# Kernel tuning notes

Hardware: AMD Instinct MI355X
Metric: run time of the kernel (lower is better)

Reference implementation:

```python
import jax, jax.numpy as jnp
import numpy as np

B, O, L, N, V, H = 4, 4, 128, 8, 256, 256  # batch, options, max_len, topN, vec_size, hidden


def _gru(x, wih, whh, bih, bhh):
    """PyTorch-style GRU (gate order r,z,n), zero init hidden. x: [b,t,d] -> [b,t,H]."""
    xg = jnp.einsum('btd,gd->btg', x, wih) + bih  # input projections for all steps
    h0 = jnp.zeros((x.shape[0], whh.shape[1]), x.dtype)

    def step(h, xt):
        hg = h @ whh.T + bhh
        xr, xz, xn = jnp.split(xt, 3, axis=-1)
        hr, hz, hn = jnp.split(hg, 3, axis=-1)
        r = jax.nn.sigmoid(xr + hr)
        z = jax.nn.sigmoid(xz + hz)
        n = jnp.tanh(xn + r * hn)
        h = (1.0 - z) * n + z * h
        return h, h

    _, ys = jax.lax.scan(step, h0, jnp.swapaxes(xg, 0, 1))
    return jnp.swapaxes(ys, 0, 1)


def setup_inputs() -> dict:
    key = jax.random.key(0)
    ks = jax.random.split(key, 19)
    r = lambda k, s, sc=1.0: jax.random.normal(k, s, jnp.float32) * sc
    w = 0.05  # weight scale
    return {
        'statement': r(ks[0], (B, L, V)),
        'answer': r(ks[1], (B, O, L, V)),
        'refs': r(ks[2], (B, O, N, L, V)),
        'ctx_wih': r(ks[3], (3 * H, V), w), 'ctx_whh': r(ks[4], (3 * H, H), w),
        'ctx_bih': r(ks[5], (3 * H,), w), 'ctx_bhh': r(ks[6], (3 * H,), w),
        'sr_wih': r(ks[7], (3 * H, H), w), 'sr_whh': r(ks[8], (3 * H, H), w),
        'sr_bih': r(ks[9], (3 * H,), w), 'sr_bhh': r(ks[10], (3 * H,), w),
        'dr_wih': r(ks[11], (3 * H, 2 * H), w), 'dr_whh': r(ks[12], (3 * H, H), w),
        'dr_bih': r(ks[13], (3 * H,), w), 'dr_bhh': r(ks[14], (3 * H,), w),
        'gate_w': r(ks[15], (1, 2 * H), w), 'gate_b': r(ks[16], (1,), w),
        'out_w': r(ks[17], (1, 4 * H), w), 'out_b': r(ks[18], (1,), w),
    }


def reference(statement, answer, refs,
              ctx_wih, ctx_whh, ctx_bih, ctx_bhh,
              sr_wih, sr_whh, sr_bih, sr_bhh,
              dr_wih, dr_whh, dr_bih, dr_bhh,
              gate_w, gate_b, out_w, out_b):
    Ls = 2 * L
    # statement = cat(question, option) per option, context-encoded (option loop vectorized)
    q = jnp.broadcast_to(statement[:, None], (B, O, L, V))
    stmt = jnp.concatenate([q, answer], axis=2)  # [B,O,Ls,V]
    stmt = _gru(stmt.reshape(B * O, Ls, V), ctx_wih, ctx_whh, ctx_bih, ctx_bhh).reshape(B, O, Ls, H)
    docs = _gru(refs.reshape(B * O * N, L, V), ctx_wih, ctx_whh, ctx_bih, ctx_bhh).reshape(B, O, N, L, H)
    # statement-doc co-attention (doc loop vectorized)
    match = jnp.einsum('bosh,bonlh->bonsl', stmt, docs)  # [B,O,N,Ls,L]
    read_sum = jnp.einsum('bonsl,bonlh->bonsh', jax.nn.softmax(match, axis=-1), docs)  # [B,O,N,Ls,H]
    doc_read = jnp.einsum('bonsl,bosh->bonlh', jax.nn.softmax(match, axis=3), stmt)    # [B,O,N,L,H]
    dri = jnp.concatenate([docs, doc_read], axis=-1)  # [B,O,N,L,2H]
    # doc-doc cross attention against all topN*L positions
    flat = dri.reshape(B, O, N * L, 2 * H)
    mm = jnp.einsum('bonld,bomd->bonlm', dri, flat)  # [B,O,N,L,N*L]
    att = jnp.einsum('bonlm,bomd->bonld', jax.nn.softmax(mm, axis=-1), flat)  # [B,O,N,L,2H]
    # reasoning GRUs + max-pool over time
    s_r = _gru(read_sum.reshape(B * O * N, Ls, H), sr_wih, sr_whh, sr_bih, sr_bhh).max(axis=1).reshape(B, O, N, H)
    d_r = _gru(att.reshape(B * O * N, L, 2 * H), dr_wih, dr_whh, dr_bih, dr_bhh).max(axis=1).reshape(B, O, N, H)
    res = jnp.concatenate([s_r, d_r], axis=-1)  # [B,O,N,2H]
    coef = jnp.einsum('bond,ed->bone', res, gate_w) + gate_b  # [B,O,N,1] (no sigmoid, as in source)
    res = coef * res
    feat = jnp.concatenate([res.max(axis=2), res.mean(axis=2)], axis=-1)  # [B,O,4H]
    out = jnp.einsum('bod,ed->boe', feat, out_w)[..., 0] + out_b  # [B,O]
    return jax.nn.softmax(out, axis=1)
```

## Files before the change

### kernel.cpp

```cpp
#include <hip/hip_runtime.h>
#include <hip/hip_bf16.h>
#include <hip/hip_fp16.h>


typedef unsigned short u16;
typedef unsigned int u32;
typedef __attribute__((ext_vector_type(8))) short short8;
typedef __attribute__((ext_vector_type(4))) float floatx4;

__device__ __forceinline__ float bf2f(u16 v) { return __uint_as_float(((u32)v) << 16); }
__device__ __forceinline__ u16 f2b(float f) {
  u32 u = __float_as_uint(f);
  return (u16)((u + 0x7fffu + ((u >> 16) & 1u)) >> 16);
}
__device__ __forceinline__ float ldf(u16 v) { return bf2f(v); }
__device__ __forceinline__ float ldf(float v) { return v; }
__device__ __forceinline__ void stf(u16* p, float v) { *p = f2b(v); }
__device__ __forceinline__ void stf(float* p, float v) { *p = v; }
__device__ __forceinline__ float ldraw(const void* p, size_t i, int isf) {
  return isf ? ((const float*)p)[i] : bf2f(((const u16*)p)[i]);
}
__device__ __forceinline__ __half2 u2h(u32 v) {
  union { u32 u; __half2 h; } c; c.u = v; return c.h;
}

__global__ void k_detect(const void* __restrict__ stmt, int* __restrict__ flag) {
  if (threadIdx.x == 0 && blockIdx.x == 0) {
    const float* f = (const float*)stmt;
    int sane = 0;
    for (int i = 0; i < 64; ++i) {
      const float a = fabsf(f[i]);
      if (a > 1e-20f && a < 1e6f) sane++;
    }
    *flag = (sane >= 48) ? 1 : 0;
  }
}

__global__ __launch_bounds__(256) void k_cvt(const void* __restrict__ in, u16* __restrict__ out,
                                             int n, const int* __restrict__ flag) {
  const int isf = *flag;
  const int i = blockIdx.x * 256 + threadIdx.x;
  if (i < n) out[i] = f2b(ldraw(in, i, isf));
}

__global__ __launch_bounds__(256) void k_gather_stmt(const void* __restrict__ statement,
                                                     const void* __restrict__ answer,
                                                     u16* __restrict__ out,
                                                     const int* __restrict__ flag) {
  const int isf = *flag;
  const int idx = blockIdx.x * 256 + threadIdx.x;
  const int v = idx & 255;
  const int s = (idx >> 8) & 255;
  const int bo = idx >> 16;
  float val;
  if (s < 128) val = ldraw(statement, (size_t)(((bo >> 2) * 128) + s) * 256 + v, isf);
  else         val = ldraw(answer, (size_t)((bo * 128) + (s - 128)) * 256 + v, isf);
  out[idx] = f2b(val);
}

__global__ __launch_bounds__(256) void k_packh(const void* __restrict__ in, u32* __restrict__ out,
                                               int total, const int* __restrict__ flag) {
  const int isf = *flag;
  const int idx = blockIdx.x * 256 + threadIdx.x;
  if (idx >= total) return;
  const int r = idx % 768;
  const int k2 = idx / 768;
  const float a = ldraw(in, (size_t)r * 256 + 2 * k2, isf);
  const float b = ldraw(in, (size_t)r * 256 + 2 * k2 + 1, isf);
  const __half2 h2 = __floats2half2_rn(a, b);
  out[(((size_t)(k2 >> 2) * 768) + r) * 4 + (k2 & 3)] = *reinterpret_cast<const u32*>(&h2);
}

#define LOADW(i) uint4 w##i = wp[(i) * 768];
#define PINW(i) asm volatile("" : "+v"(w##i.x), "+v"(w##i.y), "+v"(w##i.z), "+v"(w##i.w));
#define STEPW(i)                                                             \
  {                                                                          \
    const uint4 hv = *reinterpret_cast<const uint4*>(&hs_h[(i) * 8]);        \
    a0 = __hfma2(u2h(w##i.x), u2h(hv.x), a0);                                \
    a1 = __hfma2(u2h(w##i.y), u2h(hv.y), a1);                                \
    a2 = __hfma2(u2h(w##i.z), u2h(hv.z), a2);                                \
    a3 = __hfma2(u2h(w##i.w), u2h(hv.w), a3);                                \
  }

__global__ __attribute__((amdgpu_flat_work_group_size(768, 768), amdgpu_waves_per_eu(3, 3)))
void k_rec(
    const u16* __restrict__ xg0, const u32* __restrict__ whh0,
    const u16* __restrict__ bih0, const u16* __restrict__ bhh0,
    u16* __restrict__ oseq0, float* __restrict__ omax0, int nseq0, int T0,
    const u16* __restrict__ xg1, const u32* __restrict__ whh1,
    const u16* __restrict__ bih1, const u16* __restrict__ bhh1,
    u16* __restrict__ oseq1, float* __restrict__ omax1, int T1) {
  __shared__ __align__(16) char smem[82176];
  float* hs_f = reinterpret_cast<float*>(smem);
  __half* hs_h = reinterpret_cast<__half*>(smem + 1024);
  float* sh = reinterpret_cast<float*>(smem + 2048);
  const u16 *xg, *bih, *bhh; const u32* whh; u16* oseq; float* omax; int T, seq;
  if ((int)blockIdx.x < nseq0) {
    seq = blockIdx.x; xg = xg0; whh = whh0; bih = bih0; bhh = bhh0;
    oseq = oseq0; omax = omax0; T = T0;
  } else {
    seq = blockIdx.x - nseq0; xg = xg1; whh = whh1; bih = bih1; bhh = bhh1;
    oseq = oseq1; omax = omax1; T = T1;
  }
  const int t = threadIdx.x;
  const uint4* wp = reinterpret_cast<const uint4*>(whh) + t;
  LOADW(0)  LOADW(1)  LOADW(2)  LOADW(3)  LOADW(4)  LOADW(5)  LOADW(6)  LOADW(7)
  LOADW(8)  LOADW(9)  LOADW(10) LOADW(11) LOADW(12) LOADW(13) LOADW(14) LOADW(15)
  LOADW(16) LOADW(17) LOADW(18) LOADW(19) LOADW(20) LOADW(21) LOADW(22) LOADW(23)
  LOADW(24) LOADW(25) LOADW(26) LOADW(27) LOADW(28) LOADW(29) LOADW(30) LOADW(31)
  PINW(0)  PINW(1)  PINW(2)  PINW(3)  PINW(4)  PINW(5)  PINW(6)  PINW(7)
  PINW(8)  PINW(9)  PINW(10) PINW(11) PINW(12) PINW(13) PINW(14) PINW(15)
  PINW(16) PINW(17) PINW(18) PINW(19) PINW(20) PINW(21) PINW(22) PINW(23)
  PINW(24) PINW(25) PINW(26) PINW(27) PINW(28) PINW(29) PINW(30) PINW(31)
  const float bh = bf2f(bhh[t]);
  float bir = 0.f, biz = 0.f, bin = 0.f;
  if (t < 256) {
    bir = bf2f(bih[t]); biz = bf2f(bih[t + 256]); bin = bf2f(bih[t + 512]);
    hs_f[t] = 0.f;
    hs_h[t] = __float2half(0.f);
  }
  float vmax = -3.4e38f;
  const u16* xrow = xg + (size_t)seq * T * 768;
  for (int st = 0; st < T; ++st, xrow += 768) {
    float xr = 0.f, xz = 0.f, xn = 0.f;
    if (t < 256) {
      xr = bf2f(xrow[t]); xz = bf2f(xrow[t + 256]); xn = bf2f(xrow[t + 512]);
    }
    __syncthreads();
    __half2 a0 = __floats2half2_rn(0.f, 0.f), a1 = a0, a2 = a0, a3 = a0;
    STEPW(0)  STEPW(1)  STEPW(2)  STEPW(3)  STEPW(4)  STEPW(5)  STEPW(6)  STEPW(7)
    STEPW(8)  STEPW(9)  STEPW(10) STEPW(11) STEPW(12) STEPW(13) STEPW(14) STEPW(15)
    STEPW(16) STEPW(17) STEPW(18) STEPW(19) STEPW(20) STEPW(21) STEPW(22) STEPW(23)
    STEPW(24) STEPW(25) STEPW(26) STEPW(27) STEPW(28) STEPW(29) STEPW(30) STEPW(31)
    const float ah = (__low2float(a0) + __high2float(a0)) + (__low2float(a1) + __high2float(a1))
                   + (__low2float(a2) + __high2float(a2)) + (__low2float(a3) + __high2float(a3));
    sh[t] = ah + bh;
    __syncthreads();
    if (t < 256) {
      const float r = 1.f / (1.f + __expf(-(xr + bir + sh[t])));
      const float z = 1.f / (1.f + __expf(-(xz + biz + sh[t + 256])));
      const float n = tanhf(xn + bin + r * sh[t + 512]);
      const float hnew = (1.f - z) * n + z * hs_f[t];
      hs_f[t] = hnew;
      hs_h[t] = __float2half(hnew);
      if (oseq) oseq[(size_t)(seq * T + st) * 256 + t] = f2b(hnew);
      vmax = fmaxf(vmax, hnew);
    }
  }
  if (omax && t < 256) omax[(size_t)seq * 256 + t] = vmax;
}

template <bool BT, bool CADD, typename TA, typename TB, typename TC>
__global__ __launch_bounds__(256) void k_mgemm(
    const TA* __restrict__ Abase, int lda, long strideA, int divA,
    const TB* __restrict__ Bbase, int ldb, long strideB, int divB,
    TC* __restrict__ Cbase, int ldc, long strideC, int K) {
  const int z = blockIdx.z;
  const TA* A = Abase + (size_t)(z / divA) * strideA;
  const TB* Bp = Bbase + (size_t)(z / divB) * strideB;
  TC* C = Cbase + (size_t)z * strideC;
  const int m0 = blockIdx.y << 6, n0 = blockIdx.x << 6;
  __shared__ __align__(16) u16 As[2048];
  __shared__ __align__(16) u16 Bs[2048];
  const int t = threadIdx.x;
  const int lane = t & 63, w = t >> 6;
  floatx4 acc0 = {0.f, 0.f, 0.f, 0.f};
  floatx4 acc1 = {0.f, 0.f, 0.f, 0.f};
  floatx4 acc2 = {0.f, 0.f, 0.f, 0.f};
  floatx4 acc3 = {0.f, 0.f, 0.f, 0.f};
  const int ar = t >> 2;
  const int ac = (t & 3) << 3;
  const int adst = (((ar >> 4) << 6) | (ar & 15) | ((t & 3) << 4)) << 3;
  const int bk = t >> 3;
  const int bn = (t & 7) << 3;
  for (int k0 = 0; k0 < K; k0 += 32) {
    {
      const TA* ap = A + (size_t)(m0 + ar) * lda + (k0 + ac);
      if constexpr (sizeof(TA) == 2) {
        *reinterpret_cast<uint4*>(&As[adst]) = *reinterpret_cast<const uint4*>(ap);
      } else {
        const float4 f0 = reinterpret_cast<const float4*>(ap)[0];
        const float4 f1 = reinterpret_cast<const float4*>(ap)[1];
        u16* d = &As[adst];
        d[0] = f2b(f0.x); d[1] = f2b(f0.y); d[2] = f2b(f0.z); d[3] = f2b(f0.w);
        d[4] = f2b(f1.x); d[5] = f2b(f1.y); d[6] = f2b(f1.z); d[7] = f2b(f1.w);
      }
    }
    if constexpr (BT) {
      const TB* bp = Bp + (size_t)(n0 + ar) * ldb + (k0 + ac);
      *reinterpret_cast<uint4*>(&Bs[adst]) = *reinterpret_cast<const uint4*>(bp);
    } else {
      const TB* bp = Bp + (size_t)(k0 + bk) * ldb + (n0 + bn);
      const uint4 v = *reinterpret_cast<const uint4*>(bp);
      const u16* pv = reinterpret_cast<const u16*>(&v);
#pragma unroll
      for (int j = 0; j < 8; ++j) {
        const int n = bn + j;
        Bs[(((((n >> 4) << 6) | (n & 15) | ((bk >> 3) << 4)) << 3) | (bk & 7))] = pv[j];
      }
    }
    __syncthreads();
    const short8 af = *reinterpret_cast<const short8*>(&As[(w * 64 + lane) << 3]);
    const short8 b0 = *reinterpret_cast<const short8*>(&Bs[(lane) << 3]);
    const short8 b1 = *reinterpret_cast<const short8*>(&Bs[(64 + lane) << 3]);
    const short8 b2 = *reinterpret_cast<const short8*>(&Bs[(128 + lane) << 3]);
    const short8 b3 = *reinterpret_cast<const short8*>(&Bs[(192 + lane) << 3]);
    acc0 = __builtin_amdgcn_mfma_f32_16x16x32_bf16(af, b0, acc0, 0, 0, 0);
    acc1 = __builtin_amdgcn_mfma_f32_16x16x32_bf16(af, b1, acc1, 0, 0, 0);
    acc2 = __builtin_amdgcn_mfma_f32_16x16x32_bf16(af, b2, acc2, 0, 0, 0);
    acc3 = __builtin_amdgcn_mfma_f32_16x16x32_bf16(af, b3, acc3, 0, 0, 0);
    __syncthreads();
  }
  const int q = lane >> 4, cn = lane & 15;
  TC* crow = C + (size_t)(m0 + (w << 4) + (q << 2)) * ldc + n0 + cn;
#pragma unroll
  for (int i = 0; i < 4; ++i) {
    TC* cp = crow + (size_t)i * ldc;
    float v0 = acc0[i], v1 = acc1[i], v2 = acc2[i], v3 = acc3[i];
    if (CADD) { v0 += ldf(cp[0]); v1 += ldf(cp[16]); v2 += ldf(cp[32]); v3 += ldf(cp[48]); }
    stf(cp + 0, v0); stf(cp + 16, v1); stf(cp + 32, v2); stf(cp + 48, v3);
  }
}

template <typename TI, typename TO>
__global__ __launch_bounds__(256) void k_softmax_row(const TI* __restrict__ in,
                                                     TO* __restrict__ out, int Lrow) {
  const TI* p = in + (size_t)blockIdx.x * Lrow;
  TO* q = out + (size_t)blockIdx.x * Lrow;
  const int t = threadIdx.x;
  __shared__ float redA[4];
  __shared__ float redB[4];
  float m = -3.4e38f;
  for (int i = t; i < Lrow; i += 256) m = fmaxf(m, ldf(p[i]));
  for (int o = 32; o; o >>= 1) m = fmaxf(m, __shfl_xor(m, o, 64));
  if ((t & 63) == 0) redA[t >> 6] = m;
  __syncthreads();
  m = fmaxf(fmaxf(redA[0], redA[1]), fmaxf(redA[2], redA[3]));
  float s = 0.f;
  for (int i = t; i < Lrow; i += 256) {
    const float e = __expf(ldf(p[i]) - m);
    stf(q + i, e);
    s += e;
  }
  for (int o = 32; o; o >>= 1) s += __shfl_xor(s, o, 64);
  if ((t & 63) == 0) redB[t >> 6] = s;
  __syncthreads();
  s = redB[0] + redB[1] + redB[2] + redB[3];
  const float inv = 1.f / s;
  for (int i = t; i < Lrow; i += 256) stf(q + i, ldf(q[i]) * inv);
}

__global__ __launch_bounds__(256) void k_softmax_colT(const float* __restrict__ match,
                                                      u16* __restrict__ qT) {
  const int bon = blockIdx.x, l = blockIdx.y;
  const int t = threadIdx.x;
  __shared__ float redA[4];
  __shared__ float redB[4];
  const float x = match[((size_t)bon * 256 + t) * 128 + l];
  float m = x;
  for (int o = 32; o; o >>= 1) m = fmaxf(m, __shfl_xor(m, o, 64));
  if ((t & 63) == 0) redA[t >> 6] = m;
  __syncthreads();
  m = fmaxf(fmaxf(redA[0], redA[1]), fmaxf(redA[2], redA[3]));
  const float e = __expf(x - m);
  float s = e;
  for (int o = 32; o; o >>= 1) s += __shfl_xor(s, o, 64);
  if ((t & 63) == 0) redB[t >> 6] = s;
  __syncthreads();
  s = redB[0] + redB[1] + redB[2] + redB[3];
  qT[((size_t)bon * 128 + l) * 256 + t] = f2b(e / s);
}

__global__ __launch_bounds__(256) void k_final(
    const float* __restrict__ s_r, const float* __restrict__ d_r,
    const u16* __restrict__ gw, const u16* __restrict__ gb,
    const u16* __restrict__ ow, const u16* __restrict__ ob,
    void* __restrict__ out, const int* __restrict__ flag) {
  __shared__ float coef[128];
  __shared__ float logits[16];
  const int t = threadIdx.x;
  if (t < 128) {
    float acc = bf2f(gb[0]);
    const float* sp = s_r + (size_t)t * 256;
    const float* dp = d_r + (size_t)t * 256;
    for (int d = 0; d < 256; ++d) acc += bf2f(gw[d]) * sp[d];
    for (int d = 0; d < 256; ++d) acc += bf2f(gw[256 + d]) * dp[d];
    coef[t] = acc;
  }
  __syncthreads();
  if (t < 16) {
    float acc = bf2f(ob[0]);
    for (int d = 0; d < 512; ++d) {
      float mx = -3.4e38f, sm = 0.f;
      for (int n = 0; n < 8; ++n) {
        const int bon = t * 8 + n;
        const float base = (d < 256) ? s_r[(size_t)bon * 256 + d] : d_r[(size_t)bon * 256 + (d - 256)];
        const float v = coef[bon] * base;
        mx = fmaxf(mx, v);
        sm += v;
      }
      acc += bf2f(ow[d]) * mx + bf2f(ow[512 + d]) * (sm * 0.125f);
    }
    logits[t] = acc;
  }
  __syncthreads();
  if (t < 4) {
    const int isf = *flag;
    float m = -3.4e38f;
    for (int o = 0; o < 4; ++o) m = fmaxf(m, logits[t * 4 + o]);
    float e[4], s = 0.f;
    for (int o = 0; o < 4; ++o) { e[o] = __expf(logits[t * 4 + o] - m); s += e[o]; }
    for (int o = 0; o < 4; ++o) {
      const float v = e[o] / s;
      if (isf) ((float*)out)[t * 4 + o] = v;
      else     ((u16*)out)[t * 4 + o] = f2b(v);
    }
  }
}

extern "C" void kernel_launch(void* const* d_in, const int* in_sizes, int n_in,
                              void* d_out, int out_size, void* d_ws, size_t ws_size,
                              hipStream_t stream) {
  (void)in_sizes; (void)n_in; (void)out_size; (void)ws_size;
  const void* statement = d_in[0];
  const void* answer    = d_in[1];
  const void* refs      = d_in[2];
  const void* ctx_wih = d_in[3];
  const void* ctx_whh = d_in[4];
  const void* ctx_bih = d_in[5];
  const void* ctx_bhh = d_in[6];
  const void* sr_wih = d_in[7];
  const void* sr_whh = d_in[8];
  const void* sr_bih = d_in[9];
  const void* sr_bhh = d_in[10];
  const void* dr_wih = d_in[11];
  const void* dr_whh = d_in[12];
  const void* dr_bih = d_in[13];
  const void* dr_bhh = d_in[14];
  const void* gate_w = d_in[15];
  const void* gate_b = d_in[16];
  const void* out_w  = d_in[17];
  const void* out_b  = d_in[18];

  char* ws = (char*)d_ws;
  size_t off = 0;
  auto alloc = [&](size_t bytes) -> void* {
    void* p = ws + off;
    off += (bytes + 255) & ~(size_t)255;
    return p;
  };
  int* FLAG    = (int*)alloc(256);
  u16* CTXWIH  = (u16*)alloc((size_t)768 * 256 * 2);
  u16* SRWIH   = (u16*)alloc((size_t)768 * 256 * 2);
  u16* DRWIH   = (u16*)alloc((size_t)768 * 512 * 2);
  u32* CTXWHH2 = (u32*)alloc((size_t)128 * 768 * 4);
  u32* SRWHH2  = (u32*)alloc((size_t)128 * 768 * 4);
  u32* DRWHH2  = (u32*)alloc((size_t)128 * 768 * 4);
  u16* B_CTX_I = (u16*)alloc(768 * 2);
  u16* B_CTX_H = (u16*)alloc(768 * 2);
  u16* B_SR_I  = (u16*)alloc(768 * 2);
  u16* B_SR_H  = (u16*)alloc(768 * 2);
  u16* B_DR_I  = (u16*)alloc(768 * 2);
  u16* B_DR_H  = (u16*)alloc(768 * 2);
  u16* GW = (u16*)alloc(512 * 2);
  u16* GB = (u16*)alloc(2);
  u16* OW = (u16*)alloc(1024 * 2);
  u16* OB = (u16*)alloc(2);
  u16* STMT_H   = (u16*)alloc((size_t)16 * 256 * 256 * 2);
  u16* DOCS_H   = (u16*)alloc((size_t)128 * 128 * 256 * 2);
  u16* DOC_READ = (u16*)alloc((size_t)128 * 128 * 256 * 2);
  u16* ATT      = (u16*)alloc((size_t)128 * 128 * 512 * 2);
  float* SR_R = (float*)alloc((size_t)128 * 256 * 4);
  float* DR_R = (float*)alloc((size_t)128 * 256 * 4);
  const size_t ovl = off;
  u16* REFS_B   = (u16*)(ws + ovl);
  u16* STMT_IN  = (u16*)(ws + ovl + ((size_t)8 << 20));
  u16* XG_DOCS  = (u16*)(ws + ovl + ((size_t)16 << 20));
  u16* XG_STMT  = (u16*)(ws + ovl + ((size_t)41 << 20));
  float* MATCH  = (float*)(ws + ovl);
  u16* P_ROW    = (u16*)(ws + ovl + ((size_t)16 << 20));
  u16* MATCH_Q  = (u16*)(ws + ovl + ((size_t)24 << 20));
  u16* READ_SUM = (u16*)(ws + ovl + ((size_t)50 << 20));
  u16* XG_SR    = (u16*)(ws + ovl);
  float* MM     = (float*)(ws + ovl);
  u16* XG_DR    = (u16*)(ws + ovl);

  k_detect<<<1, 64, 0, stream>>>(statement, FLAG);

  k_gather_stmt<<<4096, 256, 0, stream>>>(statement, answer, STMT_IN, FLAG);
  k_cvt<<<16384, 256, 0, stream>>>(refs, REFS_B, 4194304, FLAG);
  k_cvt<<<768, 256, 0, stream>>>(ctx_wih, CTXWIH, 196608, FLAG);
  k_cvt<<<768, 256, 0, stream>>>(sr_wih, SRWIH, 196608, FLAG);
  k_cvt<<<1536, 256, 0, stream>>>(dr_wih, DRWIH, 393216, FLAG);
  k_packh<<<384, 256, 0, stream>>>(ctx_whh, CTXWHH2, 98304, FLAG);
  k_packh<<<384, 256, 0, stream>>>(sr_whh, SRWHH2, 98304, FLAG);
  k_packh<<<384, 256, 0, stream>>>(dr_whh, DRWHH2, 98304, FLAG);
  k_cvt<<<3, 256, 0, stream>>>(ctx_bih, B_CTX_I, 768, FLAG);
  k_cvt<<<3, 256, 0, stream>>>(ctx_bhh, B_CTX_H, 768, FLAG);
  k_cvt<<<3, 256, 0, stream>>>(sr_bih, B_SR_I, 768, FLAG);
  k_cvt<<<3, 256, 0, stream>>>(sr_bhh, B_SR_H, 768, FLAG);
  k_cvt<<<3, 256, 0, stream>>>(dr_bih, B_DR_I, 768, FLAG);
  k_cvt<<<3, 256, 0, stream>>>(dr_bhh, B_DR_H, 768, FLAG);
  k_cvt<<<2, 256, 0, stream>>>(gate_w, GW, 512, FLAG);
  k_cvt<<<1, 256, 0, stream>>>(gate_b, GB, 1, FLAG);
  k_cvt<<<4, 256, 0, stream>>>(out_w, OW, 1024, FLAG);
  k_cvt<<<1, 256, 0, stream>>>(out_b, OB, 1, FLAG);

  k_mgemm<true, false, u16, u16, u16><<<dim3(12, 64, 1), 256, 0, stream>>>(
      STMT_IN, 256, 0L, 1, CTXWIH, 256, 0L, 1, XG_STMT, 768, 0L, 256);
  k_mgemm<true, false, u16, u16, u16><<<dim3(12, 256, 1), 256, 0, stream>>>(
      REFS_B, 256, 0L, 1, CTXWIH, 256, 0L, 1, XG_DOCS, 768, 0L, 256);

  k_rec<<<144, 768, 0, stream>>>(
      XG_STMT, CTXWHH2, B_CTX_I, B_CTX_H, STMT_H, nullptr, 16, 256,
      XG_DOCS, CTXWHH2, B_CTX_I, B_CTX_H, DOCS_H, nullptr, 128);

  k_mgemm<true, false, u16, u16, float><<<dim3(2, 4, 128), 256, 0, stream>>>(
      STMT_H, 256, 65536L, 8, DOCS_H, 256, 32768L, 1, MATCH, 128, 32768L, 256);

  k_softmax_colT<<<dim3(128, 128), 256, 0, stream>>>(MATCH, MATCH_Q);
  k_softmax_row<float, u16><<<32768, 256, 0, stream>>>(MATCH, P_ROW, 128);

  k_mgemm<false, false, u16, u16, u16><<<dim3(4, 4, 128), 256, 0, stream>>>(
      P_ROW, 128, 32768L, 1, DOCS_H, 256, 32768L, 1, READ_SUM, 256, 65536L, 128);

  k_mgemm<false, false, u16, u16, u16><<<dim3(4, 2, 128), 256, 0, stream>>>(
      MATCH_Q, 256, 32768L, 1, STMT_H, 256, 65536L, 8, DOC_READ, 256, 32768L, 256);

  k_mgemm<true, false, u16, u16, u16><<<dim3(12, 512, 1), 256, 0, stream>>>(
      READ_SUM, 256, 0L, 1, SRWIH, 256, 0L, 1, XG_SR, 768, 0L, 256);

  k_rec<<<128, 768, 0, stream>>>(
      XG_SR, SRWHH2, B_SR_I, B_SR_H, nullptr, SR_R, 128, 256,
      nullptr, nullptr, nullptr, nullptr, nullptr, nullptr, 0);

  k_mgemm<true, false, u16, u16, float><<<dim3(16, 16, 16), 256, 0, stream>>>(
      DOCS_H, 256, 262144L, 1, DOCS_H, 256, 262144L, 1, MM, 1024, 1048576L, 256);
  k_mgemm<true, true, u16, u16, float><<<dim3(16, 16, 16), 256, 0, stream>>>(
      DOC_READ, 256, 262144L, 1, DOC_READ, 256, 262144L, 1, MM, 1024, 1048576L, 256);

  k_softmax_row<float, float><<<16384, 256, 0, stream>>>(MM, MM, 1024);

  k_mgemm<false, false, float, u16, u16><<<dim3(4, 16, 16), 256, 0, stream>>>(
      MM, 1024, 1048576L, 1, DOCS_H, 256, 262144L, 1, ATT, 512, 524288L, 1024);
  k_mgemm<false, false, float, u16, u16><<<dim3(4, 16, 16), 256, 0, stream>>>(
      MM, 1024, 1048576L, 1, DOC_READ, 256, 262144L, 1, ATT + 256, 512, 524288L, 1024);

  k_mgemm<true, false, u16, u16, u16><<<dim3(12, 256, 1), 256, 0, stream>>>(
      ATT, 512, 0L, 1, DRWIH, 512, 0L, 1, XG_DR, 768, 0L, 512);

  k_rec<<<128, 768, 0, stream>>>(
      XG_DR, DRWHH2, B_DR_I, B_DR_H, nullptr, DR_R, 128, 128,
      nullptr, nullptr, nullptr, nullptr, nullptr, nullptr, 0);

  k_final<<<1, 256, 0, stream>>>(SR_R, DR_R, GW, GB, OW, OB, d_out, FLAG);
}
```

Measured before the change: 1.714 ms.

## Remap GRU recurrence to 512 threads, each owning three gate rows over half the hidden dimension

The recurrent kernel now runs 512 threads instead of 768. Each thread keeps 48 packed fp16 weight vectors in registers, covering three consecutive W_hh rows over half of K. Thread pairs combine their partial sums with a lane shuffle, and the weight packing kernel is rewritten to match the new register layout. Each hidden-state vector read from LDS is now reused across three rows, which cuts LDS traffic and wave count per step. The cost is higher register pressure (192 VGPRs just for weights) and an extra shuffle and reduction on the serial per-step critical path.

```diff
diff --git a/kernel.cpp b/kernel.cpp
--- a/kernel.cpp
+++ b/kernel.cpp
@@ -61,28 +61,20 @@
 __global__ __launch_bounds__(256) void k_packh(const void* __restrict__ in, u32* __restrict__ out,
                                                int total, const int* __restrict__ flag) {
   const int isf = *flag;
-  const int idx = blockIdx.x * 256 + threadIdx.x;
-  if (idx >= total) return;
-  const int r = idx % 768;
-  const int k2 = idx / 768;
-  const float a = ldraw(in, (size_t)r * 256 + 2 * k2, isf);
-  const float b = ldraw(in, (size_t)r * 256 + 2 * k2 + 1, isf);
+  const int g = blockIdx.x * 256 + threadIdx.x;
+  if (g >= total) return;
+  const int i = g >> 11;
+  const int t = (g >> 2) & 511;
+  const int m = g & 3;
+  const int row = 3 * (t >> 1) + (i >> 4);
+  const int k = (t & 1) * 128 + (i & 15) * 8 + 2 * m;
+  const float a = ldraw(in, (size_t)row * 256 + k, isf);
+  const float b = ldraw(in, (size_t)row * 256 + k + 1, isf);
   const __half2 h2 = __floats2half2_rn(a, b);
-  out[(((size_t)(k2 >> 2) * 768) + r) * 4 + (k2 & 3)] = *reinterpret_cast<const u32*>(&h2);
-}
-
-#define LOADW(i) uint4 w##i = wp[(i) * 768];
-#define PINW(i) asm volatile("" : "+v"(w##i.x), "+v"(w##i.y), "+v"(w##i.z), "+v"(w##i.w));
-#define STEPW(i)                                                             \
-  {                                                                          \
-    const uint4 hv = *reinterpret_cast<const uint4*>(&hs_h[(i) * 8]);        \
-    a0 = __hfma2(u2h(w##i.x), u2h(hv.x), a0);                                \
-    a1 = __hfma2(u2h(w##i.y), u2h(hv.y), a1);                                \
-    a2 = __hfma2(u2h(w##i.z), u2h(hv.z), a2);                                \
-    a3 = __hfma2(u2h(w##i.w), u2h(hv.w), a3);                                \
-  }
-
-__global__ __attribute__((amdgpu_flat_work_group_size(768, 768), amdgpu_waves_per_eu(3, 3)))
+  out[g] = *reinterpret_cast<const u32*>(&h2);
+}
+
+__global__ __attribute__((amdgpu_flat_work_group_size(512, 512), amdgpu_waves_per_eu(2, 2)))
 void k_rec(
     const u16* __restrict__ xg0, const u32* __restrict__ whh0,
     const u16* __restrict__ bih0, const u16* __restrict__ bhh0,
@@ -90,10 +82,9 @@
     const u16* __restrict__ xg1, const u32* __restrict__ whh1,
     const u16* __restrict__ bih1, const u16* __restrict__ bhh1,
     u16* __restrict__ oseq1, float* __restrict__ omax1, int T1) {
-  __shared__ __align__(16) char smem[82176];
-  float* hs_f = reinterpret_cast<float*>(smem);
-  __half* hs_h = reinterpret_cast<__half*>(smem + 1024);
-  float* sh = reinterpret_cast<float*>(smem + 2048);
+  __shared__ __align__(16) float hs_f[256];
+  __shared__ __align__(16) __half hs_h[256];
+  __shared__ __align__(16) float sh[768];
   const u16 *xg, *bih, *bhh; const u32* whh; u16* oseq; float* omax; int T, seq;
   if ((int)blockIdx.x < nseq0) {
     seq = blockIdx.x; xg = xg0; whh = whh0; bih = bih0; bhh = bhh0;
@@ -103,22 +94,22 @@
     oseq = oseq1; omax = omax1; T = T1;
   }
   const int t = threadIdx.x;
+  const int p = t >> 1, kh = t & 1;
   const uint4* wp = reinterpret_cast<const uint4*>(whh) + t;
-  LOADW(0)  LOADW(1)  LOADW(2)  LOADW(3)  LOADW(4)  LOADW(5)  LOADW(6)  LOADW(7)
-  LOADW(8)  LOADW(9)  LOADW(10) LOADW(11) LOADW(12) LOADW(13) LOADW(14) LOADW(15)
-  LOADW(16) LOADW(17) LOADW(18) LOADW(19) LOADW(20) LOADW(21) LOADW(22) LOADW(23)
-  LOADW(24) LOADW(25) LOADW(26) LOADW(27) LOADW(28) LOADW(29) LOADW(30) LOADW(31)
-  PINW(0)  PINW(1)  PINW(2)  PINW(3)  PINW(4)  PINW(5)  PINW(6)  PINW(7)
-  PINW(8)  PINW(9)  PINW(10) PINW(11) PINW(12) PINW(13) PINW(14) PINW(15)
-  PINW(16) PINW(17) PINW(18) PINW(19) PINW(20) PINW(21) PINW(22) PINW(23)
-  PINW(24) PINW(25) PINW(26) PINW(27) PINW(28) PINW(29) PINW(30) PINW(31)
-  const float bh = bf2f(bhh[t]);
+  uint4 w[48];
+#pragma unroll
+  for (int i = 0; i < 48; ++i) w[i] = wp[i * 512];
+  float bh0 = 0.f, bh1 = 0.f, bh2 = 0.f;
+  if (!kh) {
+    bh0 = bf2f(bhh[3 * p]); bh1 = bf2f(bhh[3 * p + 1]); bh2 = bf2f(bhh[3 * p + 2]);
+  }
   float bir = 0.f, biz = 0.f, bin = 0.f;
   if (t < 256) {
     bir = bf2f(bih[t]); biz = bf2f(bih[t + 256]); bin = bf2f(bih[t + 512]);
     hs_f[t] = 0.f;
     hs_h[t] = __float2half(0.f);
   }
+  const uint4* hs4 = reinterpret_cast<const uint4*>(hs_h) + (kh << 4);
   float vmax = -3.4e38f;
   const u16* xrow = xg + (size_t)seq * T * 768;
   for (int st = 0; st < T; ++st, xrow += 768) {
@@ -127,14 +118,38 @@
       xr = bf2f(xrow[t]); xz = bf2f(xrow[t + 256]); xn = bf2f(xrow[t + 512]);
     }
     __syncthreads();
-    __half2 a0 = __floats2half2_rn(0.f, 0.f), a1 = a0, a2 = a0, a3 = a0;
-    STEPW(0)  STEPW(1)  STEPW(2)  STEPW(3)  STEPW(4)  STEPW(5)  STEPW(6)  STEPW(7)
-    STEPW(8)  STEPW(9)  STEPW(10) STEPW(11) STEPW(12) STEPW(13) STEPW(14) STEPW(15)
-    STEPW(16) STEPW(17) STEPW(18) STEPW(19) STEPW(20) STEPW(21) STEPW(22) STEPW(23)
-    STEPW(24) STEPW(25) STEPW(26) STEPW(27) STEPW(28) STEPW(29) STEPW(30) STEPW(31)
-    const float ah = (__low2float(a0) + __high2float(a0)) + (__low2float(a1) + __high2float(a1))
-                   + (__low2float(a2) + __high2float(a2)) + (__low2float(a3) + __high2float(a3));
-    sh[t] = ah + bh;
+#pragma unroll
+    for (int i = 0; i < 48; ++i)
+      asm volatile("" : "+v"(w[i].x), "+v"(w[i].y), "+v"(w[i].z), "+v"(w[i].w));
+    const __half2 z2 = __floats2half2_rn(0.f, 0.f);
+    __half2 a00 = z2, a01 = z2, a10 = z2, a11 = z2, a20 = z2, a21 = z2;
+#pragma unroll
+    for (int c = 0; c < 16; ++c) {
+      const uint4 hv = hs4[c];
+      a00 = __hfma2(u2h(w[c].x),      u2h(hv.x), a00);
+      a01 = __hfma2(u2h(w[c].y),      u2h(hv.y), a01);
+      a00 = __hfma2(u2h(w[c].z),      u2h(hv.z), a00);
+      a01 = __hfma2(u2h(w[c].w),      u2h(hv.w), a01);
+      a10 = __hfma2(u2h(w[16 + c].x), u2h(hv.x), a10);
+      a11 = __hfma2(u2h(w[16 + c].y), u2h(hv.y), a11);
+      a10 = __hfma2(u2h(w[16 + c].z), u2h(hv.z), a10);
+      a11 = __hfma2(u2h(w[16 + c].w), u2h(hv.w), a11);
+      a20 = __hfma2(u2h(w[32 + c].x), u2h(hv.x), a20);
+      a21 = __hfma2(u2h(w[32 + c].y), u2h(hv.y), a21);
+      a20 = __hfma2(u2h(w[32 + c].z), u2h(hv.z), a20);
+      a21 = __hfma2(u2h(w[32 + c].w), u2h(hv.w), a21);
+    }
+    float s0 = (__low2float(a00) + __high2float(a00)) + (__low2float(a01) + __high2float(a01));
+    float s1 = (__low2float(a10) + __high2float(a10)) + (__low2float(a11) + __high2float(a11));
+    float s2 = (__low2float(a20) + __high2float(a20)) + (__low2float(a21) + __high2float(a21));
+    s0 += __shfl_xor(s0, 1, 64);
+    s1 += __shfl_xor(s1, 1, 64);
+    s2 += __shfl_xor(s2, 1, 64);
+    if (!kh) {
+      sh[3 * p]     = s0 + bh0;
+      sh[3 * p + 1] = s1 + bh1;
+      sh[3 * p + 2] = s2 + bh2;
+    }
     __syncthreads();
     if (t < 256) {
       const float r = 1.f / (1.f + __expf(-(xr + bir + sh[t])));
@@ -411,7 +426,7 @@
   k_mgemm<true, false, u16, u16, u16><<<dim3(12, 256, 1), 256, 0, stream>>>(
       REFS_B, 256, 0L, 1, CTXWIH, 256, 0L, 1, XG_DOCS, 768, 0L, 256);
 
-  k_rec<<<144, 768, 0, stream>>>(
+  k_rec<<<144, 512, 0, stream>>>(
       XG_STMT, CTXWHH2, B_CTX_I, B_CTX_H, STMT_H, nullptr, 16, 256,
       XG_DOCS, CTXWHH2, B_CTX_I, B_CTX_H, DOCS_H, nullptr, 128);
 
@@ -430,7 +445,7 @@
   k_mgemm<true, false, u16, u16, u16><<<dim3(12, 512, 1), 256, 0, stream>>>(
       READ_SUM, 256, 0L, 1, SRWIH, 256, 0L, 1, XG_SR, 768, 0L, 256);
 
-  k_rec<<<128, 768, 0, stream>>>(
+  k_rec<<<128, 512, 0, stream>>>(
       XG_SR, SRWHH2, B_SR_I, B_SR_H, nullptr, SR_R, 128, 256,
       nullptr, nullptr, nullptr, nullptr, nullptr, nullptr, 0);
 
@@ -449,7 +464,7 @@
   k_mgemm<true, false, u16, u16, u16><<<dim3(12, 256, 1), 256, 0, stream>>>(
       ATT, 512, 0L, 1, DRWIH, 512, 0L, 1, XG_DR, 768, 0L, 512);
 
-  k_rec<<<128, 768, 0, stream>>>(
+  k_rec<<<128, 512, 0, stream>>>(
       XG_DR, DRWHH2, B_DR_I, B_DR_H, nullptr, DR_R, 128, 128,
       nullptr, nullptr, nullptr, nullptr, nullptr, nullptr, 0);
 
```

Measured after the change: 1.737 ms. Within noise of the previous version (+1.4%).

## Process two GRU sequences per block, streaming recurrent weights from cache

Applied to the files above, without the earlier changes.

The recurrent GRU kernel now lets each 768-thread block advance two independent sequences at once. Each weight vector is loaded once per step and applied to both hidden states, and the gate math is split across thread ranges. The old scheme pinned all recurrent weights in registers with a waves-per-EU hint. That is dropped, so weights are re-read from L1/L2 on every step, and launches shrink to roughly half as many blocks. This trades register-resident weights for fewer, busier blocks, with added per-step load latency and less parallelism across CUs.

```diff
diff --git a/kernel.cpp b/kernel.cpp
--- a/kernel.cpp
+++ b/kernel.cpp
@@ -71,83 +71,126 @@
   out[(((size_t)(k2 >> 2) * 768) + r) * 4 + (k2 & 3)] = *reinterpret_cast<const u32*>(&h2);
 }
 
-#define LOADW(i) uint4 w##i = wp[(i) * 768];
-#define PINW(i) asm volatile("" : "+v"(w##i.x), "+v"(w##i.y), "+v"(w##i.z), "+v"(w##i.w));
-#define STEPW(i)                                                             \
-  {                                                                          \
-    const uint4 hv = *reinterpret_cast<const uint4*>(&hs_h[(i) * 8]);        \
-    a0 = __hfma2(u2h(w##i.x), u2h(hv.x), a0);                                \
-    a1 = __hfma2(u2h(w##i.y), u2h(hv.y), a1);                                \
-    a2 = __hfma2(u2h(w##i.z), u2h(hv.z), a2);                                \
-    a3 = __hfma2(u2h(w##i.w), u2h(hv.w), a3);                                \
-  }
-
-__global__ __attribute__((amdgpu_flat_work_group_size(768, 768), amdgpu_waves_per_eu(3, 3)))
+#define HH1(i)                                                              \
+  {                                                                         \
+    const uint4 wv = wp[(i) * 768];                                         \
+    const uint4 hA = *reinterpret_cast<const uint4*>(&hsA_h[(i) * 8]);      \
+    a0 = __hfma2(u2h(wv.x), u2h(hA.x), a0);                                 \
+    a1 = __hfma2(u2h(wv.y), u2h(hA.y), a1);                                 \
+    a2 = __hfma2(u2h(wv.z), u2h(hA.z), a2);                                 \
+    a3 = __hfma2(u2h(wv.w), u2h(hA.w), a3);                                 \
+  }
+#define HH2(i)                                                              \
+  {                                                                         \
+    const uint4 wv = wp[(i) * 768];                                         \
+    const uint4 hA = *reinterpret_cast<const uint4*>(&hsA_h[(i) * 8]);      \
+    const uint4 hB = *reinterpret_cast<const uint4*>(&hsB_h[(i) * 8]);      \
+    a0 = __hfma2(u2h(wv.x), u2h(hA.x), a0);                                 \
+    a1 = __hfma2(u2h(wv.y), u2h(hA.y), a1);                                 \
+    a2 = __hfma2(u2h(wv.z), u2h(hA.z), a2);                                 \
+    a3 = __hfma2(u2h(wv.w), u2h(hA.w), a3);                                 \
+    b0 = __hfma2(u2h(wv.x), u2h(hB.x), b0);                                 \
+    b1 = __hfma2(u2h(wv.y), u2h(hB.y), b1);                                 \
+    b2 = __hfma2(u2h(wv.z), u2h(hB.z), b2);                                 \
+    b3 = __hfma2(u2h(wv.w), u2h(hB.w), b3);                                 \
+  }
+
+__global__ __attribute__((amdgpu_flat_work_group_size(768, 768)))
 void k_rec(
     const u16* __restrict__ xg0, const u32* __restrict__ whh0,
     const u16* __restrict__ bih0, const u16* __restrict__ bhh0,
-    u16* __restrict__ oseq0, float* __restrict__ omax0, int nseq0, int T0,
+    u16* __restrict__ oseq0, float* __restrict__ omax0, int nblk0, int S0, int T0,
     const u16* __restrict__ xg1, const u32* __restrict__ whh1,
     const u16* __restrict__ bih1, const u16* __restrict__ bhh1,
-    u16* __restrict__ oseq1, float* __restrict__ omax1, int T1) {
-  __shared__ __align__(16) char smem[82176];
-  float* hs_f = reinterpret_cast<float*>(smem);
-  __half* hs_h = reinterpret_cast<__half*>(smem + 1024);
-  float* sh = reinterpret_cast<float*>(smem + 2048);
-  const u16 *xg, *bih, *bhh; const u32* whh; u16* oseq; float* omax; int T, seq;
-  if ((int)blockIdx.x < nseq0) {
-    seq = blockIdx.x; xg = xg0; whh = whh0; bih = bih0; bhh = bhh0;
-    oseq = oseq0; omax = omax0; T = T0;
+    u16* __restrict__ oseq1, float* __restrict__ omax1, int S1, int T1) {
+  __shared__ __align__(16) float hsA_f[256];
+  __shared__ __align__(16) float hsB_f[256];
+  __shared__ __align__(16) __half hsA_h[256];
+  __shared__ __align__(16) __half hsB_h[256];
+  __shared__ __align__(16) float shA[768];
+  __shared__ __align__(16) float shB[768];
+  const u16 *xg, *bih, *bhh; const u32* whh; u16* oseq; float* omax; int T, S, blk;
+  if ((int)blockIdx.x < nblk0) {
+    blk = blockIdx.x; xg = xg0; whh = whh0; bih = bih0; bhh = bhh0;
+    oseq = oseq0; omax = omax0; T = T0; S = S0;
   } else {
-    seq = blockIdx.x - nseq0; xg = xg1; whh = whh1; bih = bih1; bhh = bhh1;
-    oseq = oseq1; omax = omax1; T = T1;
+    blk = blockIdx.x - nblk0; xg = xg1; whh = whh1; bih = bih1; bhh = bhh1;
+    oseq = oseq1; omax = omax1; T = T1; S = S1;
   }
   const int t = threadIdx.x;
+  const bool dual = (S == 2);
+  const int seqA = blk * S;
   const uint4* wp = reinterpret_cast<const uint4*>(whh) + t;
-  LOADW(0)  LOADW(1)  LOADW(2)  LOADW(3)  LOADW(4)  LOADW(5)  LOADW(6)  LOADW(7)
-  LOADW(8)  LOADW(9)  LOADW(10) LOADW(11) LOADW(12) LOADW(13) LOADW(14) LOADW(15)
-  LOADW(16) LOADW(17) LOADW(18) LOADW(19) LOADW(20) LOADW(21) LOADW(22) LOADW(23)
-  LOADW(24) LOADW(25) LOADW(26) LOADW(27) LOADW(28) LOADW(29) LOADW(30) LOADW(31)
-  PINW(0)  PINW(1)  PINW(2)  PINW(3)  PINW(4)  PINW(5)  PINW(6)  PINW(7)
-  PINW(8)  PINW(9)  PINW(10) PINW(11) PINW(12) PINW(13) PINW(14) PINW(15)
-  PINW(16) PINW(17) PINW(18) PINW(19) PINW(20) PINW(21) PINW(22) PINW(23)
-  PINW(24) PINW(25) PINW(26) PINW(27) PINW(28) PINW(29) PINW(30) PINW(31)
   const float bh = bf2f(bhh[t]);
   float bir = 0.f, biz = 0.f, bin = 0.f;
   if (t < 256) {
     bir = bf2f(bih[t]); biz = bf2f(bih[t + 256]); bin = bf2f(bih[t + 512]);
-    hs_f[t] = 0.f;
-    hs_h[t] = __float2half(0.f);
+    hsA_f[t] = 0.f; hsA_h[t] = __float2half(0.f);
+  } else if (dual && t < 512) {
+    const int e = t - 256;
+    bir = bf2f(bih[e]); biz = bf2f(bih[e + 256]); bin = bf2f(bih[e + 512]);
+    hsB_f[e] = 0.f; hsB_h[e] = __float2half(0.f);
   }
   float vmax = -3.4e38f;
-  const u16* xrow = xg + (size_t)seq * T * 768;
-  for (int st = 0; st < T; ++st, xrow += 768) {
+  const u16* xrowA = xg + (size_t)seqA * T * 768;
+  const u16* xrowB = xg + (size_t)(seqA + 1) * T * 768;
+  for (int st = 0; st < T; ++st, xrowA += 768, xrowB += 768) {
     float xr = 0.f, xz = 0.f, xn = 0.f;
     if (t < 256) {
-      xr = bf2f(xrow[t]); xz = bf2f(xrow[t + 256]); xn = bf2f(xrow[t + 512]);
+      xr = bf2f(xrowA[t]); xz = bf2f(xrowA[t + 256]); xn = bf2f(xrowA[t + 512]);
+    } else if (dual && t < 512) {
+      const int e = t - 256;
+      xr = bf2f(xrowB[e]); xz = bf2f(xrowB[e + 256]); xn = bf2f(xrowB[e + 512]);
     }
     __syncthreads();
-    __half2 a0 = __floats2half2_rn(0.f, 0.f), a1 = a0, a2 = a0, a3 = a0;
-    STEPW(0)  STEPW(1)  STEPW(2)  STEPW(3)  STEPW(4)  STEPW(5)  STEPW(6)  STEPW(7)
-    STEPW(8)  STEPW(9)  STEPW(10) STEPW(11) STEPW(12) STEPW(13) STEPW(14) STEPW(15)
-    STEPW(16) STEPW(17) STEPW(18) STEPW(19) STEPW(20) STEPW(21) STEPW(22) STEPW(23)
-    STEPW(24) STEPW(25) STEPW(26) STEPW(27) STEPW(28) STEPW(29) STEPW(30) STEPW(31)
-    const float ah = (__low2float(a0) + __high2float(a0)) + (__low2float(a1) + __high2float(a1))
+    const __half2 z2 = __floats2half2_rn(0.f, 0.f);
+    __half2 a0 = z2, a1 = z2, a2 = z2, a3 = z2;
+    __half2 b0 = z2, b1 = z2, b2 = z2, b3 = z2;
+    if (dual) {
+      HH2(0)  HH2(1)  HH2(2)  HH2(3)  HH2(4)  HH2(5)  HH2(6)  HH2(7)
+      HH2(8)  HH2(9)  HH2(10) HH2(11) HH2(12) HH2(13) HH2(14) HH2(15)
+      HH2(16) HH2(17) HH2(18) HH2(19) HH2(20) HH2(21) HH2(22) HH2(23)
+      HH2(24) HH2(25) HH2(26) HH2(27) HH2(28) HH2(29) HH2(30) HH2(31)
+    } else {
+      HH1(0)  HH1(1)  HH1(2)  HH1(3)  HH1(4)  HH1(5)  HH1(6)  HH1(7)
+      HH1(8)  HH1(9)  HH1(10) HH1(11) HH1(12) HH1(13) HH1(14) HH1(15)
+      HH1(16) HH1(17) HH1(18) HH1(19) HH1(20) HH1(21) HH1(22) HH1(23)
+      HH1(24) HH1(25) HH1(26) HH1(27) HH1(28) HH1(29) HH1(30) HH1(31)
+    }
+    const float sA = (__low2float(a0) + __high2float(a0)) + (__low2float(a1) + __high2float(a1))
                    + (__low2float(a2) + __high2float(a2)) + (__low2float(a3) + __high2float(a3));
-    sh[t] = ah + bh;
+    shA[t] = sA + bh;
+    if (dual) {
+      const float sB = (__low2float(b0) + __high2float(b0)) + (__low2float(b1) + __high2float(b1))
+                     + (__low2float(b2) + __high2float(b2)) + (__low2float(b3) + __high2float(b3));
+      shB[t] = sB + bh;
+    }
     __syncthreads();
     if (t < 256) {
-      const float r = 1.f / (1.f + __expf(-(xr + bir + sh[t])));
-      const float z = 1.f / (1.f + __expf(-(xz + biz + sh[t + 256])));
-      const float n = tanhf(xn + bin + r * sh[t + 512]);
-      const float hnew = (1.f - z) * n + z * hs_f[t];
-      hs_f[t] = hnew;
-      hs_h[t] = __float2half(hnew);
-      if (oseq) oseq[(size_t)(seq * T + st) * 256 + t] = f2b(hnew);
+      const float r = 1.f / (1.f + __expf(-(xr + bir + shA[t])));
+      const float z = 1.f / (1.f + __expf(-(xz + biz + shA[t + 256])));
+      const float n = tanhf(xn + bin + r * shA[t + 512]);
+      const float hnew = (1.f - z) * n + z * hsA_f[t];
+      hsA_f[t] = hnew;
+      hsA_h[t] = __float2half(hnew);
+      if (oseq) oseq[(size_t)(seqA * T + st) * 256 + t] = f2b(hnew);
       vmax = fmaxf(vmax, hnew);
-    }
-  }
-  if (omax && t < 256) omax[(size_t)seq * 256 + t] = vmax;
+    } else if (dual && t < 512) {
+      const int e = t - 256;
+      const float r = 1.f / (1.f + __expf(-(xr + bir + shB[e])));
+      const float z = 1.f / (1.f + __expf(-(xz + biz + shB[e + 256])));
+      const float n = tanhf(xn + bin + r * shB[e + 512]);
+      const float hnew = (1.f - z) * n + z * hsB_f[e];
+      hsB_f[e] = hnew;
+      hsB_h[e] = __float2half(hnew);
+      if (oseq) oseq[(size_t)((seqA + 1) * T + st) * 256 + e] = f2b(hnew);
+      vmax = fmaxf(vmax, hnew);
+    }
+  }
+  if (omax) {
+    if (t < 256) omax[(size_t)seqA * 256 + t] = vmax;
+    else if (dual && t < 512) omax[(size_t)(seqA + 1) * 256 + (t - 256)] = vmax;
+  }
 }
 
 template <bool BT, bool CADD, typename TA, typename TB, typename TC>
@@ -411,9 +454,9 @@
   k_mgemm<true, false, u16, u16, u16><<<dim3(12, 256, 1), 256, 0, stream>>>(
       REFS_B, 256, 0L, 1, CTXWIH, 256, 0L, 1, XG_DOCS, 768, 0L, 256);
 
-  k_rec<<<144, 768, 0, stream>>>(
-      XG_STMT, CTXWHH2, B_CTX_I, B_CTX_H, STMT_H, nullptr, 16, 256,
-      XG_DOCS, CTXWHH2, B_CTX_I, B_CTX_H, DOCS_H, nullptr, 128);
+  k_rec<<<80, 768, 0, stream>>>(
+      XG_STMT, CTXWHH2, B_CTX_I, B_CTX_H, STMT_H, nullptr, 16, 1, 256,
+      XG_DOCS, CTXWHH2, B_CTX_I, B_CTX_H, DOCS_H, nullptr, 2, 128);
 
   k_mgemm<true, false, u16, u16, float><<<dim3(2, 4, 128), 256, 0, stream>>>(
       STMT_H, 256, 65536L, 8, DOCS_H, 256, 32768L, 1, MATCH, 128, 32768L, 256);
@@ -430,9 +473,9 @@
   k_mgemm<true, false, u16, u16, u16><<<dim3(12, 512, 1), 256, 0, stream>>>(
       READ_SUM, 256, 0L, 1, SRWIH, 256, 0L, 1, XG_SR, 768, 0L, 256);
 
-  k_rec<<<128, 768, 0, stream>>>(
-      XG_SR, SRWHH2, B_SR_I, B_SR_H, nullptr, SR_R, 128, 256,
-      nullptr, nullptr, nullptr, nullptr, nullptr, nullptr, 0);
+  k_rec<<<64, 768, 0, stream>>>(
+      XG_SR, SRWHH2, B_SR_I, B_SR_H, nullptr, SR_R, 64, 2, 256,
+      nullptr, nullptr, nullptr, nullptr, nullptr, nullptr, 0, 0);
 
   k_mgemm<true, false, u16, u16, float><<<dim3(16, 16, 16), 256, 0, stream>>>(
       DOCS_H, 256, 262144L, 1, DOCS_H, 256, 262144L, 1, MM, 1024, 1048576L, 256);
@@ -449,9 +492,9 @@
   k_mgemm<true, false, u16, u16, u16><<<dim3(12, 256, 1), 256, 0, stream>>>(
       ATT, 512, 0L, 1, DRWIH, 512, 0L, 1, XG_DR, 768, 0L, 512);
 
-  k_rec<<<128, 768, 0, stream>>>(
-      XG_DR, DRWHH2, B_DR_I, B_DR_H, nullptr, DR_R, 128, 128,
-      nullptr, nullptr, nullptr, nullptr, nullptr, nullptr, 0);
+  k_rec<<<64, 768, 0, stream>>>(
+      XG_DR, DRWHH2, B_DR_I, B_DR_H, nullptr, DR_R, 64, 2, 128,
+      nullptr, nullptr, nullptr, nullptr, nullptr, nullptr, 0, 0);
 
   k_final<<<1, 256, 0, stream>>>(SR_R, DR_R, GW, GB, OW, OB, d_out, FLAG);
 }
```

Measured after the change: 3.506 ms. 2.05x slower.

## Split GRU recurrent weights between LDS and per-step global loads instead of registers

Applied to the files above, without the earlier changes.

The recurrent kernel previously kept all 32 uint4 weight chunks per thread pinned in VGPRs. Now 12 chunks are staged into shared memory once and the other 20 are reloaded from global memory (L2/cache) every time step. This frees a large number of registers, but it adds per-step LDS and global traffic to the serial critical path of the recurrence. The tradeoff only pays off if register pressure or spilling was the bottleneck before.

```diff
diff --git a/kernel.cpp b/kernel.cpp
--- a/kernel.cpp
+++ b/kernel.cpp
@@ -71,15 +71,24 @@
   out[(((size_t)(k2 >> 2) * 768) + r) * 4 + (k2 & 3)] = *reinterpret_cast<const u32*>(&h2);
 }
 
-#define LOADW(i) uint4 w##i = wp[(i) * 768];
-#define PINW(i) asm volatile("" : "+v"(w##i.x), "+v"(w##i.y), "+v"(w##i.z), "+v"(w##i.w));
-#define STEPW(i)                                                             \
+#define NLDS 12
+#define STEPG(i)                                                             \
   {                                                                          \
+    const uint4 wv = wp[(i) * 768];                                          \
     const uint4 hv = *reinterpret_cast<const uint4*>(&hs_h[(i) * 8]);        \
-    a0 = __hfma2(u2h(w##i.x), u2h(hv.x), a0);                                \
-    a1 = __hfma2(u2h(w##i.y), u2h(hv.y), a1);                                \
-    a2 = __hfma2(u2h(w##i.z), u2h(hv.z), a2);                                \
-    a3 = __hfma2(u2h(w##i.w), u2h(hv.w), a3);                                \
+    a0 = __hfma2(u2h(wv.x), u2h(hv.x), a0);                                  \
+    a1 = __hfma2(u2h(wv.y), u2h(hv.y), a1);                                  \
+    a2 = __hfma2(u2h(wv.z), u2h(hv.z), a2);                                  \
+    a3 = __hfma2(u2h(wv.w), u2h(hv.w), a3);                                  \
+  }
+#define STEPL(i)                                                             \
+  {                                                                          \
+    const uint4 wv = Wl[(i) * 768 + t];                                      \
+    const uint4 hv = *reinterpret_cast<const uint4*>(&hs_h[(i) * 8]);        \
+    a0 = __hfma2(u2h(wv.x), u2h(hv.x), a0);                                  \
+    a1 = __hfma2(u2h(wv.y), u2h(hv.y), a1);                                  \
+    a2 = __hfma2(u2h(wv.z), u2h(hv.z), a2);                                  \
+    a3 = __hfma2(u2h(wv.w), u2h(hv.w), a3);                                  \
   }
 
 __global__ __attribute__((amdgpu_flat_work_group_size(768, 768), amdgpu_waves_per_eu(3, 3)))
@@ -90,10 +99,10 @@
     const u16* __restrict__ xg1, const u32* __restrict__ whh1,
     const u16* __restrict__ bih1, const u16* __restrict__ bhh1,
     u16* __restrict__ oseq1, float* __restrict__ omax1, int T1) {
-  __shared__ __align__(16) char smem[82176];
-  float* hs_f = reinterpret_cast<float*>(smem);
-  __half* hs_h = reinterpret_cast<__half*>(smem + 1024);
-  float* sh = reinterpret_cast<float*>(smem + 2048);
+  __shared__ __align__(16) uint4 Wl[NLDS * 768];
+  __shared__ __align__(16) float hs_f[256];
+  __shared__ __align__(16) __half hs_h[256];
+  __shared__ __align__(16) float sh[768];
   const u16 *xg, *bih, *bhh; const u32* whh; u16* oseq; float* omax; int T, seq;
   if ((int)blockIdx.x < nseq0) {
     seq = blockIdx.x; xg = xg0; whh = whh0; bih = bih0; bhh = bhh0;
@@ -104,14 +113,8 @@
   }
   const int t = threadIdx.x;
   const uint4* wp = reinterpret_cast<const uint4*>(whh) + t;
-  LOADW(0)  LOADW(1)  LOADW(2)  LOADW(3)  LOADW(4)  LOADW(5)  LOADW(6)  LOADW(7)
-  LOADW(8)  LOADW(9)  LOADW(10) LOADW(11) LOADW(12) LOADW(13) LOADW(14) LOADW(15)
-  LOADW(16) LOADW(17) LOADW(18) LOADW(19) LOADW(20) LOADW(21) LOADW(22) LOADW(23)
-  LOADW(24) LOADW(25) LOADW(26) LOADW(27) LOADW(28) LOADW(29) LOADW(30) LOADW(31)
-  PINW(0)  PINW(1)  PINW(2)  PINW(3)  PINW(4)  PINW(5)  PINW(6)  PINW(7)
-  PINW(8)  PINW(9)  PINW(10) PINW(11) PINW(12) PINW(13) PINW(14) PINW(15)
-  PINW(16) PINW(17) PINW(18) PINW(19) PINW(20) PINW(21) PINW(22) PINW(23)
-  PINW(24) PINW(25) PINW(26) PINW(27) PINW(28) PINW(29) PINW(30) PINW(31)
+#pragma unroll
+  for (int i = 0; i < NLDS; ++i) Wl[i * 768 + t] = wp[i * 768];
   const float bh = bf2f(bhh[t]);
   float bir = 0.f, biz = 0.f, bin = 0.f;
   if (t < 256) {
@@ -128,10 +131,11 @@
     }
     __syncthreads();
     __half2 a0 = __floats2half2_rn(0.f, 0.f), a1 = a0, a2 = a0, a3 = a0;
-    STEPW(0)  STEPW(1)  STEPW(2)  STEPW(3)  STEPW(4)  STEPW(5)  STEPW(6)  STEPW(7)
-    STEPW(8)  STEPW(9)  STEPW(10) STEPW(11) STEPW(12) STEPW(13) STEPW(14) STEPW(15)
-    STEPW(16) STEPW(17) STEPW(18) STEPW(19) STEPW(20) STEPW(21) STEPW(22) STEPW(23)
-    STEPW(24) STEPW(25) STEPW(26) STEPW(27) STEPW(28) STEPW(29) STEPW(30) STEPW(31)
+    STEPG(12) STEPG(13) STEPG(14) STEPG(15) STEPG(16) STEPG(17) STEPG(18) STEPG(19)
+    STEPG(20) STEPG(21) STEPG(22) STEPG(23) STEPG(24) STEPG(25) STEPG(26) STEPG(27)
+    STEPG(28) STEPG(29) STEPG(30) STEPG(31)
+    STEPL(0)  STEPL(1)  STEPL(2)  STEPL(3)  STEPL(4)  STEPL(5)  STEPL(6)  STEPL(7)
+    STEPL(8)  STEPL(9)  STEPL(10) STEPL(11)
     const float ah = (__low2float(a0) + __high2float(a0)) + (__low2float(a1) + __high2float(a1))
                    + (__low2float(a2) + __high2float(a2)) + (__low2float(a3) + __high2float(a3));
     sh[t] = ah + bh;
```

New measurement: 1.758 ms. +2.6%, slower.
